# Optimization experiments

Measured on AMD Instinct MI355X. Metric: run time of the kernel, lower is better.

The kernel has to match this reference:

```python
import jax, jax.numpy as jnp
import numpy as np

D_MODEL = 1024
EXPAND = 2
D_INNER = EXPAND * D_MODEL      # 2048
D_STATE = 2
D_CONV = 4
DT_RANK = (D_MODEL + 15) // 16  # 64
BATCH, SEQ = 2, 4096
LN_EPS = 1e-5


def setup_inputs() -> dict:
    key = jax.random.key(0)
    ks = jax.random.split(key, 16)
    s = 0.02
    inp = {
        "x":       jax.random.normal(ks[0], (BATCH, SEQ, D_MODEL), jnp.float32),
        # Mamba params (torch Linear convention: W is [out, in])
        "w_in":    jax.random.normal(ks[1], (2 * D_INNER, D_MODEL), jnp.float32) * s,
        "conv_w":  jax.random.normal(ks[2], (D_INNER, 1, D_CONV), jnp.float32) * s,
        "conv_b":  jnp.zeros((D_INNER,), jnp.float32),
        "w_xproj": jax.random.normal(ks[3], (DT_RANK + 2 * D_STATE, D_INNER), jnp.float32) * s,
        "w_dt":    jax.random.normal(ks[4], (D_INNER, DT_RANK), jnp.float32) * s,
        "b_dt":    jax.random.normal(ks[5], (D_INNER,), jnp.float32) * s - 4.0,  # softplus -> small dt
        "a_log":   jnp.log(jnp.broadcast_to(jnp.arange(1, D_STATE + 1, dtype=jnp.float32), (D_INNER, D_STATE))),
        "d_skip":  jnp.ones((D_INNER,), jnp.float32),
        "w_out":   jax.random.normal(ks[6], (D_MODEL, D_INNER), jnp.float32) * s,
        # LayerNorms
        "ln1_g":   jnp.ones((D_MODEL,), jnp.float32),
        "ln1_b":   jnp.zeros((D_MODEL,), jnp.float32),
        "ln2_g":   jnp.ones((D_MODEL,), jnp.float32),
        "ln2_b":   jnp.zeros((D_MODEL,), jnp.float32),
        # FFN (Linear d->d, ReLU, Linear d->d; dropout inactive at eval)
        "ffn_w1":  jax.random.normal(ks[7], (D_MODEL, D_MODEL), jnp.float32) * s,
        "ffn_b1":  jnp.zeros((D_MODEL,), jnp.float32),
        "ffn_w2":  jax.random.normal(ks[8], (D_MODEL, D_MODEL), jnp.float32) * s,
        "ffn_b2":  jnp.zeros((D_MODEL,), jnp.float32),
    }
    return inp


def _ln(x, g, b):
    mu = x.mean(-1, keepdims=True)
    v = ((x - mu) ** 2).mean(-1, keepdims=True)
    return (x - mu) * jax.lax.rsqrt(v + LN_EPS) * g + b


def _mamba(x, w_in, conv_w, conv_b, w_xproj, w_dt, b_dt, a_log, d_skip, w_out):
    Bsz = x.shape[0]
    xz = x @ w_in.T                      # (B,L,2*D_INNER)
    xp, z = jnp.split(xz, 2, axis=-1)
    # depthwise causal conv over time
    xc = jnp.transpose(xp, (0, 2, 1))    # (B,D,L)
    xc = jax.lax.conv_general_dilated(
        xc, conv_w, window_strides=(1,), padding=[(D_CONV - 1, 0)],
        feature_group_count=D_INNER)
    xc = xc + conv_b[None, :, None]
    xp = jax.nn.silu(jnp.transpose(xc, (0, 2, 1)))   # (B,L,D)
    # input-dependent SSM params
    x_dbl = xp @ w_xproj.T               # (B,L,DT_RANK+2N)
    dt, Bm, Cm = jnp.split(x_dbl, [DT_RANK, DT_RANK + D_STATE], axis=-1)
    dt = jax.nn.softplus(dt @ w_dt.T + b_dt)          # (B,L,D)
    A = -jnp.exp(a_log)                  # (D,N)
    dA = jnp.exp(dt[..., None] * A)                  # (B,L,D,N)
    dBu = dt[..., None] * Bm[:, :, None, :] * xp[..., None]  # (B,L,D,N)

    def step(h, inp):
        da, dbu, c = inp                 # (B,D,N),(B,D,N),(B,N)
        h = da * h + dbu
        y = jnp.einsum('bdn,bn->bd', h, c)
        return h, y

    h0 = jnp.zeros((Bsz, D_INNER, D_STATE), x.dtype)
    _, ys = jax.lax.scan(step, h0, (jnp.swapaxes(dA, 0, 1),
                                    jnp.swapaxes(dBu, 0, 1),
                                    jnp.swapaxes(Cm, 0, 1)))
    y = jnp.swapaxes(ys, 0, 1)           # (B,L,D)
    y = (y + d_skip * xp) * jax.nn.silu(z)
    return y @ w_out.T                   # (B,L,d_model)


def reference(x, w_in, conv_w, conv_b, w_xproj, w_dt, b_dt, a_log, d_skip, w_out,
              ln1_g, ln1_b, ln2_g, ln2_b, ffn_w1, ffn_b1, ffn_w2, ffn_b2):
    h = x + _mamba(_ln(x, ln1_g, ln1_b), w_in, conv_w, conv_b, w_xproj,
                   w_dt, b_dt, a_log, d_skip, w_out)
    f = _ln(h, ln2_g, ln2_b)
    f = jax.nn.relu(f @ ffn_w1.T + ffn_b1) @ ffn_w2.T + ffn_b2
    return h + f
```

## Files before the change

kernel.cpp:

```cpp
#include <hip/hip_runtime.h>

typedef unsigned short u16;
typedef __bf16 bf16x8 __attribute__((ext_vector_type(8)));
typedef float f32x4 __attribute__((ext_vector_type(4)));

#define SEQ   4096
#define DM    1024
#define DI    2048
#define NTOK  8192
#define NXP   68
#define DTR   64
#define NCH   4096
#define CHUNK 64
#define NCHK  64

__device__ __forceinline__ float bf2f(u16 v) {
  union { unsigned u; float f; } x; x.u = ((unsigned)v) << 16; return x.f;
}
__device__ __forceinline__ u16 f2bf(float f) {
  unsigned u = __float_as_uint(f);
  return (u16)((u + 0x7FFFu + ((u >> 16) & 1u)) >> 16);
}

__device__ __forceinline__ void g2l16(const u16* g, u16* l) {
  __builtin_amdgcn_global_load_lds(
      (const __attribute__((address_space(1))) unsigned int*)g,
      (__attribute__((address_space(3))) unsigned int*)l, 16, 0, 0);
}

__global__ __launch_bounds__(256)
void detect_kernel(const u16* __restrict__ x, int* __restrict__ flag)
{
  __shared__ int tot;
  if (threadIdx.x == 0) tot = 0;
  __syncthreads();
  int cnt = 0;
  for (int i = threadIdx.x; i < 4096; i += 256) {
    const int e = (x[2 * i] >> 7) & 0xFF;
    if (e > 167) cnt++;
  }
  atomicAdd(&tot, cnt);
  __syncthreads();
  if (threadIdx.x == 0) flag[0] = (tot >= 8) ? 1 : 0;
}

__global__ __launch_bounds__(256)
void convert_kernel(const void* __restrict__ src, u16* __restrict__ dst, int n,
                    const int* __restrict__ flag)
{
  const int i = blockIdx.x * 256 + threadIdx.x;
  if (i < n)
    dst[i] = (*flag) ? f2bf(((const float*)src)[i]) : ((const u16*)src)[i];
}

__global__ __launch_bounds__(256)
void convert_small_kernel(const void* s0, const void* s1, const void* s2,
                          const void* s3, const void* s4, const void* s5,
                          const void* s6, const void* s7, const void* s8,
                          const void* s9, const void* s10,
                          u16* __restrict__ dst, const int* __restrict__ flag)
{
  const int i = blockIdx.x * 256 + threadIdx.x;
  if (i >= 24576) return;
  const void* src; int off;
  if      (i < 8192)  { src = s0;  off = i; }
  else if (i < 10240) { src = s1;  off = i - 8192; }
  else if (i < 12288) { src = s2;  off = i - 10240; }
  else if (i < 16384) { src = s3;  off = i - 12288; }
  else if (i < 18432) { src = s4;  off = i - 16384; }
  else if (i < 19456) { src = s5;  off = i - 18432; }
  else if (i < 20480) { src = s6;  off = i - 19456; }
  else if (i < 21504) { src = s7;  off = i - 20480; }
  else if (i < 22528) { src = s8;  off = i - 21504; }
  else if (i < 23552) { src = s9;  off = i - 22528; }
  else                { src = s10; off = i - 23552; }
  dst[i] = (*flag) ? f2bf(((const float*)src)[off]) : ((const u16*)src)[off];
}

template<bool DUAL>
__global__ __launch_bounds__(256)
void ln_kernel(const void* __restrict__ xin, const u16* __restrict__ gw,
               const u16* __restrict__ bw, u16* __restrict__ outp,
               const int* __restrict__ flag)
{
  const int row = blockIdx.x;
  const int tid = threadIdx.x;
  const bool isf32 = DUAL ? (*flag != 0) : true;
  const float* xf = (const float*)xin;
  const u16*   xb = (const u16*)xin;
  float v[4];
#pragma unroll
  for (int k = 0; k < 4; ++k) {
    size_t idx = (size_t)row * DM + tid + k * 256;
    v[k] = isf32 ? xf[idx] : bf2f(xb[idx]);
  }
  float s = v[0] + v[1] + v[2] + v[3];
  float s2 = v[0]*v[0] + v[1]*v[1] + v[2]*v[2] + v[3]*v[3];
#pragma unroll
  for (int off = 32; off > 0; off >>= 1) {
    s  += __shfl_down(s,  off);
    s2 += __shfl_down(s2, off);
  }
  __shared__ float red[8];
  const int wv = tid >> 6, lane = tid & 63;
  if (lane == 0) { red[wv] = s; red[4 + wv] = s2; }
  __syncthreads();
  if (tid == 0) {
    float ts = red[0] + red[1] + red[2] + red[3];
    float t2 = red[4] + red[5] + red[6] + red[7];
    float mu = ts * (1.f / DM);
    float var = t2 * (1.f / DM) - mu * mu;
    red[0] = mu; red[1] = rsqrtf(var + 1e-5f);
  }
  __syncthreads();
  const float mu = red[0], rs = red[1];
#pragma unroll
  for (int k = 0; k < 4; ++k) {
    int col = tid + k * 256;
    size_t idx = (size_t)row * DM + col;
    outp[idx] = f2bf((v[k] - mu) * rs * bf2f(gw[col]) + bf2f(bw[col]));
  }
}

template<int EPI, int LNBX>
__global__ __launch_bounds__(256, 2)
void gemm_kernel(const u16* __restrict__ A, const u16* __restrict__ B,
                 int M, int N, int K,
                 const u16* __restrict__ bias, const u16* __restrict__ addbf,
                 const float* __restrict__ addf, const int* __restrict__ dtflag,
                 void* __restrict__ Cp)
{
  __shared__ __align__(16) u16 sA[2][128 * 32];
  __shared__ __align__(16) u16 sB[2][128 * 32];
  const int tid = threadIdx.x;
  const int b = blockIdx.x;
  const int xcd = b & 7;
  const int kk = b >> 3;
  const int bx = kk & ((1 << LNBX) - 1);
  const int by = xcd * 8 + (kk >> LNBX);
  const int m0 = by * 128;
  const int n0 = bx * 128;
  const int lane = tid & 63;
  const int wv = tid >> 6;
  const int wm = (wv & 1) * 64;
  const int wn = (wv >> 1) * 64;
  const int r = lane & 15;
  const int q = lane >> 4;

  const int pr = lane >> 2;
  const int pk = (lane & 3) * 8;
  u16* lA0[2] = { &sA[0][(wv * 2 + 0) * 512], &sA[1][(wv * 2 + 0) * 512] };
  u16* lA1[2] = { &sA[0][(wv * 2 + 1) * 512], &sA[1][(wv * 2 + 1) * 512] };
  u16* lB0[2] = { &sB[0][(wv * 2 + 0) * 512], &sB[1][(wv * 2 + 0) * 512] };
  u16* lB1[2] = { &sB[0][(wv * 2 + 1) * 512], &sB[1][(wv * 2 + 1) * 512] };
  const u16* gA0 = A + (size_t)(m0 + wv * 32 + pr) * K + pk;
  const u16* gA1 = gA0 + (size_t)16 * K;
  const u16* gB0 = B + (size_t)(n0 + wv * 32 + pr) * K + pk;
  const u16* gB1 = gB0 + (size_t)16 * K;

  const int fl = (EPI == 3 || EPI == 5) ? *dtflag : 0;

  f32x4 acc[4][4];
#pragma unroll
  for (int i = 0; i < 4; ++i)
#pragma unroll
    for (int j = 0; j < 4; ++j)
#pragma unroll
      for (int t = 0; t < 4; ++t) acc[i][j][t] = 0.f;

  g2l16(gA0, lA0[0]); g2l16(gA1, lA1[0]);
  g2l16(gB0, lB0[0]); g2l16(gB1, lB1[0]);

  const int nk = K >> 5;
  for (int kt = 0; kt < nk; ++kt) {
    const int cur = kt & 1;
    __syncthreads();
    bf16x8 af[4], bfr[4];
#pragma unroll
    for (int i = 0; i < 4; ++i)
      af[i] = *reinterpret_cast<const bf16x8*>(&sA[cur][(wm + i * 16 + r) * 32 + q * 8]);
#pragma unroll
    for (int j = 0; j < 4; ++j)
      bfr[j] = *reinterpret_cast<const bf16x8*>(&sB[cur][(wn + j * 16 + r) * 32 + q * 8]);
    if (kt + 1 < nk) {
      gA0 += 32; gA1 += 32; gB0 += 32; gB1 += 32;
      g2l16(gA0, lA0[cur ^ 1]); g2l16(gA1, lA1[cur ^ 1]);
      g2l16(gB0, lB0[cur ^ 1]); g2l16(gB1, lB1[cur ^ 1]);
    }
#pragma unroll
    for (int i = 0; i < 4; ++i)
#pragma unroll
      for (int j = 0; j < 4; ++j)
        acc[i][j] = __builtin_amdgcn_mfma_f32_16x16x32_bf16(af[i], bfr[j], acc[i][j], 0, 0, 0);
  }

#pragma unroll
  for (int i = 0; i < 4; ++i) {
#pragma unroll
    for (int j = 0; j < 4; ++j) {
#pragma unroll
      for (int t = 0; t < 4; ++t) {
        const int row = m0 + wm + i * 16 + q * 4 + t;
        const int col = n0 + wn + j * 16 + r;
        const size_t idx = (size_t)row * N + col;
        float v = acc[i][j][t];
        if (EPI == 1) {
          ((u16*)Cp)[idx] = f2bf(v);
        } else if (EPI == 2) {
          v += bf2f(bias[col]);
          v = (v > 15.f) ? v : __logf(1.f + __expf(v));
          ((u16*)Cp)[idx] = f2bf(v);
        } else if (EPI == 3) {
          v += fl ? addf[idx] : bf2f(addbf[idx]);
          ((float*)Cp)[idx] = v;
        } else if (EPI == 4) {
          v += bf2f(bias[col]);
          ((u16*)Cp)[idx] = f2bf(fmaxf(v, 0.f));
        } else {
          v += bf2f(bias[col]) + addf[idx];
          if (fl) ((float*)Cp)[idx] = v;
          else    ((u16*)Cp)[idx] = f2bf(v);
        }
      }
    }
  }
}

__global__ __launch_bounds__(256, 2)
void xproj_splitk(const u16* __restrict__ A, const u16* __restrict__ B,
                  float* __restrict__ part)
{
  __shared__ __align__(16) u16 sA[2][128 * 32];
  __shared__ __align__(16) u16 sB[2][128 * 32];
  const int tid = threadIdx.x;
  const int kz = blockIdx.x;
  const int m0 = blockIdx.y * 128;
  const int kbase = kz * 256;
  const int lane = tid & 63;
  const int wv = tid >> 6;
  const int wm = (wv & 1) * 64;
  const int wn = (wv >> 1) * 64;
  const int r = lane & 15;
  const int q = lane >> 4;
  const int pr = lane >> 2;
  const int pk = (lane & 3) * 8;

  u16* lA0[2] = { &sA[0][(wv * 2 + 0) * 512], &sA[1][(wv * 2 + 0) * 512] };
  u16* lA1[2] = { &sA[0][(wv * 2 + 1) * 512], &sA[1][(wv * 2 + 1) * 512] };
  u16* lB0[2] = { &sB[0][(wv * 2 + 0) * 512], &sB[1][(wv * 2 + 0) * 512] };
  u16* lB1[2] = { &sB[0][(wv * 2 + 1) * 512], &sB[1][(wv * 2 + 1) * 512] };
  int br0 = wv * 32 + pr;      if (br0 > 67) br0 = 67;
  int br1 = wv * 32 + 16 + pr; if (br1 > 67) br1 = 67;
  const u16* gA0 = A + (size_t)(m0 + wv * 32 + pr) * DI + kbase + pk;
  const u16* gA1 = gA0 + (size_t)16 * DI;
  const u16* gB0 = B + (size_t)br0 * DI + kbase + pk;
  const u16* gB1 = B + (size_t)br1 * DI + kbase + pk;

  f32x4 acc[4][4];
#pragma unroll
  for (int i = 0; i < 4; ++i)
#pragma unroll
    for (int j = 0; j < 4; ++j)
#pragma unroll
      for (int t = 0; t < 4; ++t) acc[i][j][t] = 0.f;

  g2l16(gA0, lA0[0]); g2l16(gA1, lA1[0]);
  g2l16(gB0, lB0[0]); g2l16(gB1, lB1[0]);

  for (int kt = 0; kt < 8; ++kt) {
    const int cur = kt & 1;
    __syncthreads();
    bf16x8 af[4], bfr[4];
#pragma unroll
    for (int i = 0; i < 4; ++i)
      af[i] = *reinterpret_cast<const bf16x8*>(&sA[cur][(wm + i * 16 + r) * 32 + q * 8]);
#pragma unroll
    for (int j = 0; j < 4; ++j)
      bfr[j] = *reinterpret_cast<const bf16x8*>(&sB[cur][(wn + j * 16 + r) * 32 + q * 8]);
    if (kt + 1 < 8) {
      gA0 += 32; gA1 += 32; gB0 += 32; gB1 += 32;
      g2l16(gA0, lA0[cur ^ 1]); g2l16(gA1, lA1[cur ^ 1]);
      g2l16(gB0, lB0[cur ^ 1]); g2l16(gB1, lB1[cur ^ 1]);
    }
#pragma unroll
    for (int i = 0; i < 4; ++i)
#pragma unroll
      for (int j = 0; j < 4; ++j)
        acc[i][j] = __builtin_amdgcn_mfma_f32_16x16x32_bf16(af[i], bfr[j], acc[i][j], 0, 0, 0);
  }

#pragma unroll
  for (int i = 0; i < 4; ++i)
#pragma unroll
    for (int j = 0; j < 4; ++j)
#pragma unroll
      for (int t = 0; t < 4; ++t) {
        const int row = m0 + wm + i * 16 + q * 4 + t;
        const int col = wn + j * 16 + r;
        if (col < NXP)
          part[((size_t)kz * NTOK + row) * NXP + col] = acc[i][j][t];
      }
}

__global__ __launch_bounds__(256)
void xreduce_kernel(const float* __restrict__ part, u16* __restrict__ dtraw,
                    float* __restrict__ bc)
{
  const int i = blockIdx.x * 256 + threadIdx.x;
  if (i >= NTOK * NXP) return;
  const int row = i / NXP, col = i - row * NXP;
  float s = 0.f;
#pragma unroll
  for (int z = 0; z < 8; ++z) s += part[(size_t)z * NTOK * NXP + i];
  if (col < DTR) dtraw[(size_t)row * DTR + col] = f2bf(s);
  else           bc[row * 4 + (col - DTR)] = s;
}

__global__ __launch_bounds__(256)
void conv_silu_kernel(const u16* __restrict__ xp, const u16* __restrict__ cw,
                      const u16* __restrict__ cb, u16* __restrict__ u)
{
  const int i = blockIdx.x * 256 + threadIdx.x;
  const int d = i & (DI - 1);
  const int token = i >> 11;
  const int t = token & (SEQ - 1);
  float acc = bf2f(cb[d]);
#pragma unroll
  for (int j = 0; j < 4; ++j) {
    const int tt = t - 3 + j;
    if (tt >= 0)
      acc += bf2f(cw[d * 4 + j]) * bf2f(xp[(size_t)(token - 3 + j) * DI + d]);
  }
  const float sg = 1.f / (1.f + __expf(-acc));
  u[i] = f2bf(acc * sg);
}

__global__ __launch_bounds__(256)
void scan_pass1(const u16* __restrict__ dtb, const u16* __restrict__ ub,
                const float* __restrict__ bc, const u16* __restrict__ a_log,
                float* __restrict__ S, float* __restrict__ hf0, float* __restrict__ hf1)
{
  const int g = blockIdx.x * 256 + threadIdx.x;
  const int ch = g & (NCH - 1);
  const int c = g >> 12;
  const int b = ch >> 11;
  const int d = ch & (DI - 1);
  const float A0 = -__expf(bf2f(a_log[d * 2 + 0]));
  const float A1 = -__expf(bf2f(a_log[d * 2 + 1]));
  float h0 = 0.f, h1 = 0.f, s = 0.f;
  const int row0 = b * SEQ + c * CHUNK;
  for (int i = 0; i < CHUNK; ++i) {
    const size_t row = row0 + i;
    const float dt = bf2f(dtb[row * DI + d]);
    const float uu = bf2f(ub[row * DI + d]);
    const float B0 = bc[row * 4 + 0];
    const float B1 = bc[row * 4 + 1];
    const float dtu = dt * uu;
    h0 = __expf(A0 * dt) * h0 + dtu * B0;
    h1 = __expf(A1 * dt) * h1 + dtu * B1;
    s += dt;
  }
  S[g] = s; hf0[g] = h0; hf1[g] = h1;
}

__global__ __launch_bounds__(256)
void scan_pass2(const float* __restrict__ S, const float* __restrict__ hf0,
                const float* __restrict__ hf1, const u16* __restrict__ a_log,
                float* __restrict__ hi0, float* __restrict__ hi1)
{
  const int ch = blockIdx.x * 256 + threadIdx.x;
  const int d = ch & (DI - 1);
  const float A0 = -__expf(bf2f(a_log[d * 2 + 0]));
  const float A1 = -__expf(bf2f(a_log[d * 2 + 1]));
  float h0 = 0.f, h1 = 0.f;
  for (int c = 0; c < NCHK; ++c) {
    const int g = c * NCH + ch;
    hi0[g] = h0; hi1[g] = h1;
    const float s = S[g];
    h0 = __expf(A0 * s) * h0 + hf0[g];
    h1 = __expf(A1 * s) * h1 + hf1[g];
  }
}

__global__ __launch_bounds__(256)
void scan_pass3(const u16* __restrict__ dtb, const u16* __restrict__ ub,
                const float* __restrict__ bc, const u16* __restrict__ zbuf,
                const u16* __restrict__ a_log, const u16* __restrict__ d_skip,
                const float* __restrict__ hi0, const float* __restrict__ hi1,
                u16* __restrict__ yb)
{
  const int g = blockIdx.x * 256 + threadIdx.x;
  const int ch = g & (NCH - 1);
  const int c = g >> 12;
  const int b = ch >> 11;
  const int d = ch & (DI - 1);
  const float A0 = -__expf(bf2f(a_log[d * 2 + 0]));
  const float A1 = -__expf(bf2f(a_log[d * 2 + 1]));
  const float dsk = bf2f(d_skip[d]);
  float h0 = hi0[g], h1 = hi1[g];
  const int row0 = b * SEQ + c * CHUNK;
  for (int i = 0; i < CHUNK; ++i) {
    const size_t row = row0 + i;
    const float dt = bf2f(dtb[row * DI + d]);
    const float uu = bf2f(ub[row * DI + d]);
    const float B0 = bc[row * 4 + 0];
    const float B1 = bc[row * 4 + 1];
    const float C0 = bc[row * 4 + 2];
    const float C1 = bc[row * 4 + 3];
    const float dtu = dt * uu;
    h0 = __expf(A0 * dt) * h0 + dtu * B0;
    h1 = __expf(A1 * dt) * h1 + dtu * B1;
    const float y = h0 * C0 + h1 * C1;
    const float z = bf2f(zbuf[row * DI + d]);
    const float sz = z / (1.f + __expf(-z));
    yb[row * DI + d] = f2bf((y + dsk * uu) * sz);
  }
}

extern "C" void kernel_launch(void* const* d_in, const int* in_sizes, int n_in,
                              void* d_out, int out_size, void* d_ws, size_t ws_size,
                              hipStream_t stream)
{
  const void* x       = d_in[0];
  const void* w_in    = d_in[1];
  const void* conv_w  = d_in[2];
  const void* conv_b  = d_in[3];
  const void* w_xproj = d_in[4];
  const void* w_dt    = d_in[5];
  const void* b_dt    = d_in[6];
  const void* a_log   = d_in[7];
  const void* d_skip  = d_in[8];
  const void* w_out   = d_in[9];
  const void* ln1_g   = d_in[10];
  const void* ln1_b   = d_in[11];
  const void* ln2_g   = d_in[12];
  const void* ln2_b   = d_in[13];
  const void* ffn_w1  = d_in[14];
  const void* ffn_b1  = d_in[15];
  const void* ffn_w2  = d_in[16];
  const void* ffn_b2  = d_in[17];
  char* ws = (char*)d_ws;

  const size_t o_flag  = 0;
  const size_t o_small = 256;
  const size_t o_cwout = o_small + 65536;
  const size_t o_cff1  = o_cwout + (size_t)DM * DI * 2;
  const size_t o_cff2  = o_cff1  + (size_t)DM * DM * 2;
  const size_t o_cxp   = o_cff2  + (size_t)DM * DM * 2;
  const size_t o_cwdt  = o_cxp   + (size_t)NXP * DI * 2;
  const size_t o_xn    = 9437184;
  const size_t o_xp    = o_xn + (size_t)NTOK * DM * 2;
  const size_t o_z     = o_xp + (size_t)NTOK * DI * 2;
  const size_t o_u     = o_z  + (size_t)NTOK * DI * 2;
  const size_t o_bc    = o_u  + (size_t)NTOK * DI * 2;
  const size_t o_S     = o_bc + (size_t)NTOK * 4 * 4 + 2097152;
  const size_t o_hf0   = o_S   + (size_t)NCHK * NCH * 4;
  const size_t o_hf1   = o_hf0 + (size_t)NCHK * NCH * 4;
  const size_t o_hi0   = o_hf1 + (size_t)NCHK * NCH * 4;
  const size_t o_hi1   = o_hi0 + (size_t)NCHK * NCH * 4;

  int*   flagp   = (int*)(ws + o_flag);
  u16*   csmall  = (u16*)(ws + o_small);
  u16*   c_convw = csmall +     0;
  u16*   c_convb = csmall +  8192;
  u16*   c_bdt   = csmall + 10240;
  u16*   c_alog  = csmall + 12288;
  u16*   c_dskip = csmall + 16384;
  u16*   c_ln1g  = csmall + 18432;
  u16*   c_ln1b  = csmall + 19456;
  u16*   c_ln2g  = csmall + 20480;
  u16*   c_ln2b  = csmall + 21504;
  u16*   c_fb1   = csmall + 22528;
  u16*   c_fb2   = csmall + 23552;
  u16*   c_wout  = (u16*)(ws + o_cwout);
  u16*   c_ff1   = (u16*)(ws + o_cff1);
  u16*   c_ff2   = (u16*)(ws + o_cff2);
  u16*   c_xproj = (u16*)(ws + o_cxp);
  u16*   c_wdt   = (u16*)(ws + o_cwdt);
  u16*   c_win   = (u16*)(ws + o_u);
  u16*   xn      = (u16*)(ws + o_xn);
  u16*   xp      = (u16*)(ws + o_xp);
  u16*   zb      = (u16*)(ws + o_z);
  u16*   u       = (u16*)(ws + o_u);
  float* part    = (float*)(ws + o_xp);
  u16*   dtraw   = (u16*)(ws + o_xn);
  u16*   dtb     = xp;
  u16*   yb      = xp;
  float* bc      = (float*)(ws + o_bc);
  float* S       = (float*)(ws + o_S);
  float* hf0     = (float*)(ws + o_hf0);
  float* hf1     = (float*)(ws + o_hf1);
  float* hi0     = (float*)(ws + o_hi0);
  float* hi1     = (float*)(ws + o_hi1);
  float* h       = (float*)(ws + o_z);
  u16*   hn      = (u16*)(ws + o_xn);
  u16*   f1      = (u16*)(ws + o_u);

  const dim3 blk(256);

  detect_kernel<<<1, blk, 0, stream>>>((const u16*)x, flagp);
  convert_kernel<<<(2 * DI * DM) / 256, blk, 0, stream>>>(w_in, c_win, 2 * DI * DM, flagp);
  convert_kernel<<<(NXP * DI + 255) / 256, blk, 0, stream>>>(w_xproj, c_xproj, NXP * DI, flagp);
  convert_kernel<<<(DI * DTR) / 256, blk, 0, stream>>>(w_dt, c_wdt, DI * DTR, flagp);
  convert_kernel<<<(DM * DI) / 256, blk, 0, stream>>>(w_out, c_wout, DM * DI, flagp);
  convert_kernel<<<(DM * DM) / 256, blk, 0, stream>>>(ffn_w1, c_ff1, DM * DM, flagp);
  convert_kernel<<<(DM * DM) / 256, blk, 0, stream>>>(ffn_w2, c_ff2, DM * DM, flagp);
  convert_small_kernel<<<96, blk, 0, stream>>>(conv_w, conv_b, b_dt, a_log, d_skip,
                                               ln1_g, ln1_b, ln2_g, ln2_b, ffn_b1, ffn_b2,
                                               csmall, flagp);

  ln_kernel<true><<<NTOK, blk, 0, stream>>>(x, c_ln1g, c_ln1b, xn, flagp);
  gemm_kernel<1, 4><<<1024, blk, 0, stream>>>(xn, c_win, NTOK, DI, DM,
                                              nullptr, nullptr, nullptr, flagp, xp);
  gemm_kernel<1, 4><<<1024, blk, 0, stream>>>(xn, c_win + (size_t)DI * DM, NTOK, DI, DM,
                                              nullptr, nullptr, nullptr, flagp, zb);
  conv_silu_kernel<<<NTOK * DI / 256, blk, 0, stream>>>(xp, c_convw, c_convb, u);
  xproj_splitk<<<dim3(8, 64), blk, 0, stream>>>(u, c_xproj, part);
  xreduce_kernel<<<(NTOK * NXP + 255) / 256, blk, 0, stream>>>(part, dtraw, bc);
  gemm_kernel<2, 4><<<1024, blk, 0, stream>>>(dtraw, c_wdt, NTOK, DI, DTR,
                                              c_bdt, nullptr, nullptr, flagp, dtb);
  scan_pass1<<<NCHK * NCH / 256, blk, 0, stream>>>(dtb, u, bc, c_alog, S, hf0, hf1);
  scan_pass2<<<NCH / 256, blk, 0, stream>>>(S, hf0, hf1, c_alog, hi0, hi1);
  scan_pass3<<<NCHK * NCH / 256, blk, 0, stream>>>(dtb, u, bc, zb, c_alog, c_dskip,
                                                   hi0, hi1, yb);
  gemm_kernel<3, 3><<<512, blk, 0, stream>>>(yb, c_wout, NTOK, DM, DI,
                                             nullptr, (const u16*)x, (const float*)x,
                                             flagp, h);
  ln_kernel<false><<<NTOK, blk, 0, stream>>>(h, c_ln2g, c_ln2b, hn, flagp);
  gemm_kernel<4, 3><<<512, blk, 0, stream>>>(hn, c_ff1, NTOK, DM, DM,
                                             c_fb1, nullptr, nullptr, flagp, f1);
  gemm_kernel<5, 3><<<512, blk, 0, stream>>>(f1, c_ff2, NTOK, DM, DM,
                                             c_fb2, nullptr, h, flagp, d_out);
}
```

Measured before the change: 517.7 us.

## Vectorize LN, conv and scan kernels, fuse in-proj GEMMs, halve scan chunk

Several independent changes land at once. The two in-projection GEMMs merge into one launch that writes xp and z through a split epilogue. LayerNorm now handles two rows per block, and LayerNorm, depthwise conv (with transposed weights) and both scan passes use vectorized 8/4-wide loads and stores. The scan chunk shrinks from 64 to 32, which doubles the number of chunks for more parallelism but gives the sequential pass2 more work. Weight conversion kernels exit early when inputs are already bf16, and GEMMs then read the raw weight pointers directly; scan buffers also reuse the xn workspace.

```diff
diff --git a/kernel.cpp b/kernel.cpp
--- a/kernel.cpp
+++ b/kernel.cpp
@@ -3,6 +3,9 @@
 typedef unsigned short u16;
 typedef __bf16 bf16x8 __attribute__((ext_vector_type(8)));
 typedef float f32x4 __attribute__((ext_vector_type(4)));
+typedef float f32x2 __attribute__((ext_vector_type(2)));
+typedef u16 u16x4 __attribute__((ext_vector_type(4)));
+typedef u16 u16x8 __attribute__((ext_vector_type(8)));
 
 #define SEQ   4096
 #define DM    1024
@@ -11,8 +14,8 @@
 #define NXP   68
 #define DTR   64
 #define NCH   4096
-#define CHUNK 64
-#define NCHK  64
+#define CHUNK 32
+#define NCHK  128
 
 __device__ __forceinline__ float bf2f(u16 v) {
   union { unsigned u; float f; } x; x.u = ((unsigned)v) << 16; return x.f;
@@ -48,9 +51,9 @@
 void convert_kernel(const void* __restrict__ src, u16* __restrict__ dst, int n,
                     const int* __restrict__ flag)
 {
+  if (*flag == 0) return;
   const int i = blockIdx.x * 256 + threadIdx.x;
-  if (i < n)
-    dst[i] = (*flag) ? f2bf(((const float*)src)[i]) : ((const u16*)src)[i];
+  if (i < n) dst[i] = f2bf(((const float*)src)[i]);
 }
 
 __global__ __launch_bounds__(256)
@@ -62,8 +65,9 @@
 {
   const int i = blockIdx.x * 256 + threadIdx.x;
   if (i >= 24576) return;
-  const void* src; int off;
-  if      (i < 8192)  { src = s0;  off = i; }
+  const void* src; int off; int dsti = i;
+  if      (i < 8192)  { src = s0;  off = i;
+                        dsti = (off & 3) * DI + (off >> 2); }
   else if (i < 10240) { src = s1;  off = i - 8192; }
   else if (i < 12288) { src = s2;  off = i - 10240; }
   else if (i < 16384) { src = s3;  off = i - 12288; }
@@ -74,7 +78,7 @@
   else if (i < 22528) { src = s8;  off = i - 21504; }
   else if (i < 23552) { src = s9;  off = i - 22528; }
   else                { src = s10; off = i - 23552; }
-  dst[i] = (*flag) ? f2bf(((const float*)src)[off]) : ((const u16*)src)[off];
+  dst[dsti] = (*flag) ? f2bf(((const float*)src)[off]) : ((const u16*)src)[off];
 }
 
 template<bool DUAL>
@@ -83,55 +87,65 @@
                const u16* __restrict__ bw, u16* __restrict__ outp,
                const int* __restrict__ flag)
 {
-  const int row = blockIdx.x;
   const int tid = threadIdx.x;
+  const int sub = tid >> 7;
+  const int col0 = (tid & 127) * 8;
+  const int row = blockIdx.x * 2 + sub;
   const bool isf32 = DUAL ? (*flag != 0) : true;
-  const float* xf = (const float*)xin;
-  const u16*   xb = (const u16*)xin;
-  float v[4];
-#pragma unroll
-  for (int k = 0; k < 4; ++k) {
-    size_t idx = (size_t)row * DM + tid + k * 256;
-    v[k] = isf32 ? xf[idx] : bf2f(xb[idx]);
-  }
-  float s = v[0] + v[1] + v[2] + v[3];
-  float s2 = v[0]*v[0] + v[1]*v[1] + v[2]*v[2] + v[3]*v[3];
+  float v[8];
+  if (isf32) {
+    const float* xf = (const float*)xin + (size_t)row * DM + col0;
+    f32x4 a = *(const f32x4*)xf, b2 = *(const f32x4*)(xf + 4);
+#pragma unroll
+    for (int k = 0; k < 4; ++k) { v[k] = a[k]; v[4 + k] = b2[k]; }
+  } else {
+    u16x8 xb = *(const u16x8*)((const u16*)xin + (size_t)row * DM + col0);
+#pragma unroll
+    for (int k = 0; k < 8; ++k) v[k] = bf2f(xb[k]);
+  }
+  float s = 0.f, s2 = 0.f;
+#pragma unroll
+  for (int k = 0; k < 8; ++k) { s += v[k]; s2 += v[k] * v[k]; }
 #pragma unroll
   for (int off = 32; off > 0; off >>= 1) {
     s  += __shfl_down(s,  off);
     s2 += __shfl_down(s2, off);
   }
-  __shared__ float red[8];
-  const int wv = tid >> 6, lane = tid & 63;
-  if (lane == 0) { red[wv] = s; red[4 + wv] = s2; }
+  __shared__ float red[4], red2[4];
+  __shared__ f32x2 stat[2];
+  const int wv = tid >> 6;
+  if ((tid & 63) == 0) { red[wv] = s; red2[wv] = s2; }
   __syncthreads();
-  if (tid == 0) {
-    float ts = red[0] + red[1] + red[2] + red[3];
-    float t2 = red[4] + red[5] + red[6] + red[7];
+  if ((tid & 127) == 0) {
+    float ts = red[sub * 2] + red[sub * 2 + 1];
+    float t2 = red2[sub * 2] + red2[sub * 2 + 1];
     float mu = ts * (1.f / DM);
     float var = t2 * (1.f / DM) - mu * mu;
-    red[0] = mu; red[1] = rsqrtf(var + 1e-5f);
+    stat[sub] = f32x2{mu, rsqrtf(var + 1e-5f)};
   }
   __syncthreads();
-  const float mu = red[0], rs = red[1];
-#pragma unroll
-  for (int k = 0; k < 4; ++k) {
-    int col = tid + k * 256;
-    size_t idx = (size_t)row * DM + col;
-    outp[idx] = f2bf((v[k] - mu) * rs * bf2f(gw[col]) + bf2f(bw[col]));
-  }
+  const float mu = stat[sub][0], rs = stat[sub][1];
+  u16x8 gv = *(const u16x8*)(gw + col0), bv = *(const u16x8*)(bw + col0);
+  u16x8 o;
+#pragma unroll
+  for (int k = 0; k < 8; ++k)
+    o[k] = f2bf((v[k] - mu) * rs * bf2f(gv[k]) + bf2f(bv[k]));
+  *(u16x8*)(outp + (size_t)row * DM + col0) = o;
 }
 
 template<int EPI, int LNBX>
 __global__ __launch_bounds__(256, 2)
-void gemm_kernel(const u16* __restrict__ A, const u16* __restrict__ B,
+void gemm_kernel(const u16* __restrict__ A, const u16* __restrict__ Bc,
+                 const u16* __restrict__ Braw,
                  int M, int N, int K,
                  const u16* __restrict__ bias, const u16* __restrict__ addbf,
                  const float* __restrict__ addf, const int* __restrict__ dtflag,
-                 void* __restrict__ Cp)
+                 void* __restrict__ Cp, void* __restrict__ Cp2)
 {
   __shared__ __align__(16) u16 sA[2][128 * 32];
   __shared__ __align__(16) u16 sB[2][128 * 32];
+  const int fl = *dtflag;
+  const u16* __restrict__ B = fl ? Bc : Braw;
   const int tid = threadIdx.x;
   const int b = blockIdx.x;
   const int xcd = b & 7;
@@ -158,8 +172,6 @@
   const u16* gB0 = B + (size_t)(n0 + wv * 32 + pr) * K + pk;
   const u16* gB1 = gB0 + (size_t)16 * K;
 
-  const int fl = (EPI == 3 || EPI == 5) ? *dtflag : 0;
-
   f32x4 acc[4][4];
 #pragma unroll
   for (int i = 0; i < 4; ++i)
@@ -202,24 +214,30 @@
       for (int t = 0; t < 4; ++t) {
         const int row = m0 + wm + i * 16 + q * 4 + t;
         const int col = n0 + wn + j * 16 + r;
-        const size_t idx = (size_t)row * N + col;
         float v = acc[i][j][t];
-        if (EPI == 1) {
-          ((u16*)Cp)[idx] = f2bf(v);
-        } else if (EPI == 2) {
-          v += bf2f(bias[col]);
-          v = (v > 15.f) ? v : __logf(1.f + __expf(v));
-          ((u16*)Cp)[idx] = f2bf(v);
-        } else if (EPI == 3) {
-          v += fl ? addf[idx] : bf2f(addbf[idx]);
-          ((float*)Cp)[idx] = v;
-        } else if (EPI == 4) {
-          v += bf2f(bias[col]);
-          ((u16*)Cp)[idx] = f2bf(fmaxf(v, 0.f));
+        if (EPI == 6) {
+          const size_t rb = (size_t)row * DI;
+          if (col < DI) ((u16*)Cp)[rb + col] = f2bf(v);
+          else          ((u16*)Cp2)[rb + col - DI] = f2bf(v);
         } else {
-          v += bf2f(bias[col]) + addf[idx];
-          if (fl) ((float*)Cp)[idx] = v;
-          else    ((u16*)Cp)[idx] = f2bf(v);
+          const size_t idx = (size_t)row * N + col;
+          if (EPI == 1) {
+            ((u16*)Cp)[idx] = f2bf(v);
+          } else if (EPI == 2) {
+            v += bf2f(bias[col]);
+            v = (v > 15.f) ? v : __logf(1.f + __expf(v));
+            ((u16*)Cp)[idx] = f2bf(v);
+          } else if (EPI == 3) {
+            v += fl ? addf[idx] : bf2f(addbf[idx]);
+            ((float*)Cp)[idx] = v;
+          } else if (EPI == 4) {
+            v += bf2f(bias[col]);
+            ((u16*)Cp)[idx] = f2bf(fmaxf(v, 0.f));
+          } else {
+            v += bf2f(bias[col]) + addf[idx];
+            if (fl) ((float*)Cp)[idx] = v;
+            else    ((u16*)Cp)[idx] = f2bf(v);
+          }
         }
       }
     }
@@ -227,11 +245,14 @@
 }
 
 __global__ __launch_bounds__(256, 2)
-void xproj_splitk(const u16* __restrict__ A, const u16* __restrict__ B,
+void xproj_splitk(const u16* __restrict__ A, const u16* __restrict__ Bc,
+                  const u16* __restrict__ Braw, const int* __restrict__ dtflag,
                   float* __restrict__ part)
 {
   __shared__ __align__(16) u16 sA[2][128 * 32];
   __shared__ __align__(16) u16 sB[2][128 * 32];
+  const int fl = *dtflag;
+  const u16* __restrict__ B = fl ? Bc : Braw;
   const int tid = threadIdx.x;
   const int kz = blockIdx.x;
   const int m0 = blockIdx.y * 128;
@@ -317,22 +338,33 @@
 }
 
 __global__ __launch_bounds__(256)
-void conv_silu_kernel(const u16* __restrict__ xp, const u16* __restrict__ cw,
+void conv_silu_kernel(const u16* __restrict__ xp, const u16* __restrict__ cwT,
                       const u16* __restrict__ cb, u16* __restrict__ u)
 {
-  const int i = blockIdx.x * 256 + threadIdx.x;
-  const int d = i & (DI - 1);
-  const int token = i >> 11;
+  const int token = blockIdx.x;
   const int t = token & (SEQ - 1);
-  float acc = bf2f(cb[d]);
+  const int d0 = threadIdx.x * 8;
+  const ptrdiff_t base = (ptrdiff_t)token * DI + d0;
+  float acc[8];
+  u16x8 cbv = *(const u16x8*)(cb + d0);
+#pragma unroll
+  for (int k = 0; k < 8; ++k) acc[k] = bf2f(cbv[k]);
 #pragma unroll
   for (int j = 0; j < 4; ++j) {
-    const int tt = t - 3 + j;
-    if (tt >= 0)
-      acc += bf2f(cw[d * 4 + j]) * bf2f(xp[(size_t)(token - 3 + j) * DI + d]);
-  }
-  const float sg = 1.f / (1.f + __expf(-acc));
-  u[i] = f2bf(acc * sg);
+    if (t - 3 + j >= 0) {
+      u16x8 xv = *(const u16x8*)(xp + base + (ptrdiff_t)(j - 3) * DI);
+      u16x8 wv = *(const u16x8*)(cwT + j * DI + d0);
+#pragma unroll
+      for (int k = 0; k < 8; ++k) acc[k] += bf2f(wv[k]) * bf2f(xv[k]);
+    }
+  }
+  u16x8 o;
+#pragma unroll
+  for (int k = 0; k < 8; ++k) {
+    const float sg = 1.f / (1.f + __expf(-acc[k]));
+    o[k] = f2bf(acc[k] * sg);
+  }
+  *(u16x8*)(u + base) = o;
 }
 
 __global__ __launch_bounds__(256)
@@ -340,27 +372,40 @@
                 const float* __restrict__ bc, const u16* __restrict__ a_log,
                 float* __restrict__ S, float* __restrict__ hf0, float* __restrict__ hf1)
 {
-  const int g = blockIdx.x * 256 + threadIdx.x;
-  const int ch = g & (NCH - 1);
-  const int c = g >> 12;
-  const int b = ch >> 11;
-  const int d = ch & (DI - 1);
-  const float A0 = -__expf(bf2f(a_log[d * 2 + 0]));
-  const float A1 = -__expf(bf2f(a_log[d * 2 + 1]));
-  float h0 = 0.f, h1 = 0.f, s = 0.f;
+  const int g4 = blockIdx.x * 256 + threadIdx.x;
+  const int chg = g4 & (NCH / 4 - 1);
+  const int c = g4 >> 10;
+  const int ch0 = chg * 4;
+  const int b = ch0 >> 11;
+  const int d0 = ch0 & (DI - 1);
+  u16x8 av = *(const u16x8*)(a_log + d0 * 2);
+  float A0[4], A1[4];
+#pragma unroll
+  for (int k = 0; k < 4; ++k) {
+    A0[k] = -__expf(bf2f(av[2 * k]));
+    A1[k] = -__expf(bf2f(av[2 * k + 1]));
+  }
+  float h0[4] = {0.f, 0.f, 0.f, 0.f}, h1[4] = {0.f, 0.f, 0.f, 0.f};
+  float s[4] = {0.f, 0.f, 0.f, 0.f};
   const int row0 = b * SEQ + c * CHUNK;
   for (int i = 0; i < CHUNK; ++i) {
     const size_t row = row0 + i;
-    const float dt = bf2f(dtb[row * DI + d]);
-    const float uu = bf2f(ub[row * DI + d]);
-    const float B0 = bc[row * 4 + 0];
-    const float B1 = bc[row * 4 + 1];
-    const float dtu = dt * uu;
-    h0 = __expf(A0 * dt) * h0 + dtu * B0;
-    h1 = __expf(A1 * dt) * h1 + dtu * B1;
-    s += dt;
-  }
-  S[g] = s; hf0[g] = h0; hf1[g] = h1;
+    u16x4 dtv = *(const u16x4*)(dtb + row * DI + d0);
+    u16x4 uv  = *(const u16x4*)(ub + row * DI + d0);
+    f32x2 Bv = *(const f32x2*)(bc + row * 4);
+#pragma unroll
+    for (int k = 0; k < 4; ++k) {
+      const float dt = bf2f(dtv[k]);
+      const float dtu = dt * bf2f(uv[k]);
+      h0[k] = __expf(A0[k] * dt) * h0[k] + dtu * Bv[0];
+      h1[k] = __expf(A1[k] * dt) * h1[k] + dtu * Bv[1];
+      s[k] += dt;
+    }
+  }
+  const size_t g0 = (size_t)c * NCH + ch0;
+  *(f32x4*)(S + g0)   = f32x4{s[0], s[1], s[2], s[3]};
+  *(f32x4*)(hf0 + g0) = f32x4{h0[0], h0[1], h0[2], h0[3]};
+  *(f32x4*)(hf1 + g0) = f32x4{h1[0], h1[1], h1[2], h1[3]};
 }
 
 __global__ __launch_bounds__(256)
@@ -374,7 +419,7 @@
   const float A1 = -__expf(bf2f(a_log[d * 2 + 1]));
   float h0 = 0.f, h1 = 0.f;
   for (int c = 0; c < NCHK; ++c) {
-    const int g = c * NCH + ch;
+    const size_t g = (size_t)c * NCH + ch;
     hi0[g] = h0; hi1[g] = h1;
     const float s = S[g];
     h0 = __expf(A0 * s) * h0 + hf0[g];
@@ -389,31 +434,48 @@
                 const float* __restrict__ hi0, const float* __restrict__ hi1,
                 u16* __restrict__ yb)
 {
-  const int g = blockIdx.x * 256 + threadIdx.x;
-  const int ch = g & (NCH - 1);
-  const int c = g >> 12;
-  const int b = ch >> 11;
-  const int d = ch & (DI - 1);
-  const float A0 = -__expf(bf2f(a_log[d * 2 + 0]));
-  const float A1 = -__expf(bf2f(a_log[d * 2 + 1]));
-  const float dsk = bf2f(d_skip[d]);
-  float h0 = hi0[g], h1 = hi1[g];
+  const int g4 = blockIdx.x * 256 + threadIdx.x;
+  const int chg = g4 & (NCH / 4 - 1);
+  const int c = g4 >> 10;
+  const int ch0 = chg * 4;
+  const int b = ch0 >> 11;
+  const int d0 = ch0 & (DI - 1);
+  u16x8 av = *(const u16x8*)(a_log + d0 * 2);
+  u16x4 dkv = *(const u16x4*)(d_skip + d0);
+  float A0[4], A1[4], dsk[4];
+#pragma unroll
+  for (int k = 0; k < 4; ++k) {
+    A0[k] = -__expf(bf2f(av[2 * k]));
+    A1[k] = -__expf(bf2f(av[2 * k + 1]));
+    dsk[k] = bf2f(dkv[k]);
+  }
+  const size_t g0 = (size_t)c * NCH + ch0;
+  f32x4 h0v = *(const f32x4*)(hi0 + g0);
+  f32x4 h1v = *(const f32x4*)(hi1 + g0);
+  float h0[4], h1[4];
+#pragma unroll
+  for (int k = 0; k < 4; ++k) { h0[k] = h0v[k]; h1[k] = h1v[k]; }
   const int row0 = b * SEQ + c * CHUNK;
   for (int i = 0; i < CHUNK; ++i) {
     const size_t row = row0 + i;
-    const float dt = bf2f(dtb[row * DI + d]);
-    const float uu = bf2f(ub[row * DI + d]);
-    const float B0 = bc[row * 4 + 0];
-    const float B1 = bc[row * 4 + 1];
-    const float C0 = bc[row * 4 + 2];
-    const float C1 = bc[row * 4 + 3];
-    const float dtu = dt * uu;
-    h0 = __expf(A0 * dt) * h0 + dtu * B0;
-    h1 = __expf(A1 * dt) * h1 + dtu * B1;
-    const float y = h0 * C0 + h1 * C1;
-    const float z = bf2f(zbuf[row * DI + d]);
-    const float sz = z / (1.f + __expf(-z));
-    yb[row * DI + d] = f2bf((y + dsk * uu) * sz);
+    u16x4 dtv = *(const u16x4*)(dtb + row * DI + d0);
+    u16x4 uv  = *(const u16x4*)(ub + row * DI + d0);
+    u16x4 zv  = *(const u16x4*)(zbuf + row * DI + d0);
+    f32x4 bcv = *(const f32x4*)(bc + row * 4);
+    u16x4 o;
+#pragma unroll
+    for (int k = 0; k < 4; ++k) {
+      const float dt = bf2f(dtv[k]);
+      const float uu = bf2f(uv[k]);
+      const float dtu = dt * uu;
+      h0[k] = __expf(A0[k] * dt) * h0[k] + dtu * bcv[0];
+      h1[k] = __expf(A1[k] * dt) * h1[k] + dtu * bcv[1];
+      const float y = h0[k] * bcv[2] + h1[k] * bcv[3];
+      const float z = bf2f(zv[k]);
+      const float sz = z / (1.f + __expf(-z));
+      o[k] = f2bf((y + dsk[k] * uu) * sz);
+    }
+    *(u16x4*)(yb + row * DI + d0) = o;
   }
 }
 
@@ -453,15 +515,16 @@
   const size_t o_z     = o_xp + (size_t)NTOK * DI * 2;
   const size_t o_u     = o_z  + (size_t)NTOK * DI * 2;
   const size_t o_bc    = o_u  + (size_t)NTOK * DI * 2;
-  const size_t o_S     = o_bc + (size_t)NTOK * 4 * 4 + 2097152;
-  const size_t o_hf0   = o_S   + (size_t)NCHK * NCH * 4;
-  const size_t o_hf1   = o_hf0 + (size_t)NCHK * NCH * 4;
-  const size_t o_hi0   = o_hf1 + (size_t)NCHK * NCH * 4;
-  const size_t o_hi1   = o_hi0 + (size_t)NCHK * NCH * 4;
+  const size_t SCN = (size_t)NCHK * NCH * 4;
+  const size_t o_S   = o_xn + 0 * SCN;
+  const size_t o_hf0 = o_xn + 1 * SCN;
+  const size_t o_hf1 = o_xn + 2 * SCN;
+  const size_t o_hi0 = o_xn + 3 * SCN;
+  const size_t o_hi1 = o_xn + 4 * SCN;
 
   int*   flagp   = (int*)(ws + o_flag);
   u16*   csmall  = (u16*)(ws + o_small);
-  u16*   c_convw = csmall +     0;
+  u16*   c_cwT   = csmall +     0;
   u16*   c_convb = csmall +  8192;
   u16*   c_bdt   = csmall + 10240;
   u16*   c_alog  = csmall + 12288;
@@ -509,26 +572,30 @@
                                                ln1_g, ln1_b, ln2_g, ln2_b, ffn_b1, ffn_b2,
                                                csmall, flagp);
 
-  ln_kernel<true><<<NTOK, blk, 0, stream>>>(x, c_ln1g, c_ln1b, xn, flagp);
-  gemm_kernel<1, 4><<<1024, blk, 0, stream>>>(xn, c_win, NTOK, DI, DM,
-                                              nullptr, nullptr, nullptr, flagp, xp);
-  gemm_kernel<1, 4><<<1024, blk, 0, stream>>>(xn, c_win + (size_t)DI * DM, NTOK, DI, DM,
-                                              nullptr, nullptr, nullptr, flagp, zb);
-  conv_silu_kernel<<<NTOK * DI / 256, blk, 0, stream>>>(xp, c_convw, c_convb, u);
-  xproj_splitk<<<dim3(8, 64), blk, 0, stream>>>(u, c_xproj, part);
+  ln_kernel<true><<<NTOK / 2, blk, 0, stream>>>(x, c_ln1g, c_ln1b, xn, flagp);
+  gemm_kernel<6, 5><<<2048, blk, 0, stream>>>(xn, c_win, (const u16*)w_in,
+                                              NTOK, 2 * DI, DM,
+                                              nullptr, nullptr, nullptr, flagp, xp, zb);
+  conv_silu_kernel<<<NTOK, blk, 0, stream>>>(xp, c_cwT, c_convb, u);
+  xproj_splitk<<<dim3(8, 64), blk, 0, stream>>>(u, c_xproj, (const u16*)w_xproj,
+                                                flagp, part);
   xreduce_kernel<<<(NTOK * NXP + 255) / 256, blk, 0, stream>>>(part, dtraw, bc);
-  gemm_kernel<2, 4><<<1024, blk, 0, stream>>>(dtraw, c_wdt, NTOK, DI, DTR,
-                                              c_bdt, nullptr, nullptr, flagp, dtb);
-  scan_pass1<<<NCHK * NCH / 256, blk, 0, stream>>>(dtb, u, bc, c_alog, S, hf0, hf1);
+  gemm_kernel<2, 4><<<1024, blk, 0, stream>>>(dtraw, c_wdt, (const u16*)w_dt,
+                                              NTOK, DI, DTR,
+                                              c_bdt, nullptr, nullptr, flagp, dtb, nullptr);
+  scan_pass1<<<NCHK * NCH / 4 / 256, blk, 0, stream>>>(dtb, u, bc, c_alog, S, hf0, hf1);
   scan_pass2<<<NCH / 256, blk, 0, stream>>>(S, hf0, hf1, c_alog, hi0, hi1);
-  scan_pass3<<<NCHK * NCH / 256, blk, 0, stream>>>(dtb, u, bc, zb, c_alog, c_dskip,
-                                                   hi0, hi1, yb);
-  gemm_kernel<3, 3><<<512, blk, 0, stream>>>(yb, c_wout, NTOK, DM, DI,
+  scan_pass3<<<NCHK * NCH / 4 / 256, blk, 0, stream>>>(dtb, u, bc, zb, c_alog, c_dskip,
+                                                       hi0, hi1, yb);
+  gemm_kernel<3, 3><<<512, blk, 0, stream>>>(yb, c_wout, (const u16*)w_out,
+                                             NTOK, DM, DI,
                                              nullptr, (const u16*)x, (const float*)x,
-                                             flagp, h);
-  ln_kernel<false><<<NTOK, blk, 0, stream>>>(h, c_ln2g, c_ln2b, hn, flagp);
-  gemm_kernel<4, 3><<<512, blk, 0, stream>>>(hn, c_ff1, NTOK, DM, DM,
-                                             c_fb1, nullptr, nullptr, flagp, f1);
-  gemm_kernel<5, 3><<<512, blk, 0, stream>>>(f1, c_ff2, NTOK, DM, DM,
-                                             c_fb2, nullptr, h, flagp, d_out);
-}
+                                             flagp, h, nullptr);
+  ln_kernel<false><<<NTOK / 2, blk, 0, stream>>>(h, c_ln2g, c_ln2b, hn, flagp);
+  gemm_kernel<4, 3><<<512, blk, 0, stream>>>(hn, c_ff1, (const u16*)ffn_w1,
+                                             NTOK, DM, DM,
+                                             c_fb1, nullptr, nullptr, flagp, f1, nullptr);
+  gemm_kernel<5, 3><<<512, blk, 0, stream>>>(f1, c_ff2, (const u16*)ffn_w2,
+                                             NTOK, DM, DM,
+                                             c_fb2, nullptr, h, flagp, d_out, nullptr);
+}
```

New measurement: 503.8 us. -2.7%, faster.
